# Optimization experiments

Measured on AMD Instinct MI355X. Metric: run time of the kernel, lower is better.

Reference implementation:

```python
import jax, jax.numpy as jnp
import numpy as np

LN_EPS = 1e-5

def _layer_norm(x, gamma, beta):
    mu = jnp.mean(x, axis=-1, keepdims=True)
    var = jnp.mean(jnp.square(x - mu), axis=-1, keepdims=True)
    return (x - mu) * jax.lax.rsqrt(var + LN_EPS) * gamma + beta

def setup_inputs() -> dict:
    key = jax.random.key(0)
    ks = jax.random.split(key, 10)
    B, S, D_IN = 8, 2048, 1024
    H1, H2, C = 2048, 1024, 64
    s1 = 1.0 / np.sqrt(D_IN)
    s2 = 1.0 / np.sqrt(H1)
    s3 = 1.0 / np.sqrt(H2)
    return {
        "embeddings": jax.random.normal(ks[0], (B, S, D_IN), jnp.float32),
        "prior_evidence": jax.random.normal(ks[1], (B, C), jnp.float32),
        "W1": jax.random.uniform(ks[2], (D_IN, H1), jnp.float32, -s1, s1),
        "b1": jnp.zeros((H1,), jnp.float32),
        "g1": jnp.ones((H1,), jnp.float32),
        "beta1": jnp.zeros((H1,), jnp.float32),
        "W2": jax.random.uniform(ks[3], (H1, H2), jnp.float32, -s2, s2),
        "b2": jnp.zeros((H2,), jnp.float32),
        "g2": jnp.ones((H2,), jnp.float32),
        "beta2": jnp.zeros((H2,), jnp.float32),
        "Wh": jax.random.uniform(ks[4], (H2, C), jnp.float32, -s3, s3),
        "bh": jnp.zeros((C,), jnp.float32),
        "and_gate": jnp.ones((C,), jnp.float32),
        "or_gate": jnp.ones((C,), jnp.float32),
    }

def reference(embeddings, prior_evidence, W1, b1, g1, beta1, W2, b2, g2, beta2, Wh, bh, and_gate, or_gate):
    # feature extractor: Linear -> ReLU -> Dropout(eval: identity) -> LayerNorm, x2
    h = _layer_norm(jax.nn.relu(embeddings @ W1 + b1), g1, beta1)
    features = _layer_norm(jax.nn.relu(h @ W2 + b2), g2, beta2)  # [B,S,H2]
    d = features.shape[-1]
    scores = jnp.einsum('bsd,btd->bst', features, features) / jnp.sqrt(jnp.float32(d))
    attention_weights = jax.nn.softmax(scores, axis=-1)          # [B,S,S]
    attended = jnp.einsum('bst,btd->bsd', attention_weights, features)
    logits = attended @ Wh + bh                                   # [B,S,C]
    sig_l = jax.nn.sigmoid(logits)
    sig_p = jax.nn.sigmoid(prior_evidence)[:, None, :]            # [B,1,C] broadcasts
    and_ev = jnp.minimum(sig_l, sig_p) * and_gate
    or_ev = jnp.maximum(sig_l, sig_p) * or_gate
    logits = jnp.log((and_ev + or_ev) / 2 + 1e-10)
    return (logits, attention_weights)
```

## Files before the change

### kernel.cpp

```cpp
#include <hip/hip_runtime.h>

typedef unsigned short u16;
typedef __bf16 bf16x8 __attribute__((ext_vector_type(8)));
typedef float f32x4 __attribute__((ext_vector_type(4)));

__device__ __forceinline__ u16 f2bf(float f) {
    unsigned u = __float_as_uint(f);
    u = (u + 0x7FFFu + ((u >> 16) & 1u)) >> 16;
    return (u16)u;
}
__device__ __forceinline__ float bf2f(u16 h) {
    return __uint_as_float(((unsigned)h) << 16);
}

__device__ __forceinline__ void gld16(const u16* g, u16* l) {
    __builtin_amdgcn_global_load_lds((const __attribute__((address_space(1))) void*)g,
                                     (__attribute__((address_space(3))) void*)l, 16, 0, 0);
}

__device__ __forceinline__ int swz(int row, int col) {
    return ((row >> 4) * 2 + (col >> 5)) * 512 + (row & 15) * 32 +
           ((col & 31) ^ ((row & 8) ? 16 : 0));
}

__global__ __launch_bounds__(256) void cvt_kernel(const float* __restrict__ in,
                                                  u16* __restrict__ out, long n) {
    long i = ((long)blockIdx.x * blockDim.x + threadIdx.x) * 4;
    if (i + 3 < n) {
        float4 v = *(const float4*)&in[i];
        __align__(8) u16 r[4] = {f2bf(v.x), f2bf(v.y), f2bf(v.z), f2bf(v.w)};
        *(int2*)&out[i] = *(const int2*)r;
    }
}

template <int INF32>
__global__ __launch_bounds__(256) void transpose_to_bf16(const void* __restrict__ in,
                                                         u16* __restrict__ out, int R, int C,
                                                         long inB, long outB) {
    __shared__ float tile[32][33];
    const long zi = (long)blockIdx.z * inB;
    const long zo = (long)blockIdx.z * outB;
    const int c0 = blockIdx.x * 32, r0 = blockIdx.y * 32;
    const int tx = threadIdx.x & 31;
    const int ty = threadIdx.x >> 5;
#pragma unroll
    for (int i = 0; i < 32; i += 8) {
        long idx = zi + (long)(r0 + ty + i) * C + c0 + tx;
        float v = INF32 ? ((const float*)in)[idx] : bf2f(((const u16*)in)[idx]);
        tile[ty + i][tx] = v;
    }
    __syncthreads();
#pragma unroll
    for (int i = 0; i < 32; i += 8) {
        out[zo + (long)(c0 + ty + i) * R + r0 + tx] = f2bf(tile[tx][ty + i]);
    }
}

template <int OUTBF>
__global__ __launch_bounds__(512, 2) void gemm_nt(const u16* __restrict__ A,
                                                  const u16* __restrict__ Bm,
                                                  void* __restrict__ Cout, int M, int N, int K,
                                                  long sA, long sB, long sC,
                                                  const float* __restrict__ bias, int relu,
                                                  float scale, int symm) {
    int bx, by, zz;
    if (symm) {
        const int q = gridDim.x >> 3;
        const int orig = blockIdx.x;
        const int wgid = (orig & 7) * q + (orig >> 3);
        const int NB = N >> 8;
        const int nTri = (NB * (NB + 1)) >> 1;
        zz = wgid / nTri;
        int t = wgid - zz * nTri;
        by = 0;
        int rem = NB;
        while (t >= rem) {
            t -= rem;
            --rem;
            ++by;
        }
        bx = by + t;
    } else {
        const int nx = gridDim.x;
        const int nwg = nx * gridDim.y;
        const int orig = blockIdx.y * nx + blockIdx.x;
        const int q = nwg >> 3, r = nwg & 7, xcd = orig & 7, o8 = orig >> 3;
        const int wgid = (xcd < r ? xcd * (q + 1) : r * (q + 1) + (xcd - r) * q) + o8;
        bx = wgid % nx;
        by = wgid / nx;
        zz = blockIdx.z;
    }

    __shared__ __align__(16) u16 As[2][256 * 64];
    __shared__ __align__(16) u16 Bs[2][256 * 64];
    const int tid = threadIdx.x;
    const int lane = tid & 63;
    const int wid = tid >> 6;
    const int wr = wid >> 2;
    const int wc = wid & 3;
    const int l15 = lane & 15, lg = lane >> 4;
    const long zA = (long)zz * sA;
    const long zB = (long)zz * sB;
    const long zC = (long)zz * sC;
    const int m0 = by * 256, n0 = bx * 256;
    const u16* Ab = A + zA + (long)m0 * K;
    const u16* Bb = Bm + zB + (long)n0 * K;
    const int nt = K >> 6;

    f32x4 acc[8][4] = {};

    auto stage = [&](int t, int b) {
#pragma unroll
        for (int i = 0; i < 4; ++i) {
            const int c = i * 512 + tid;
            const int s = c >> 6, r = (c >> 2) & 15;
            const int row = (s >> 1) * 16 + r;
            const int col = (s & 1) * 32 + (((c & 3) * 8) ^ ((r & 8) ? 16 : 0));
            gld16(Ab + (long)row * K + t * 64 + col, &As[b][c * 8]);
        }
#pragma unroll
        for (int i = 0; i < 4; ++i) {
            const int c = i * 512 + tid;
            const int s = c >> 6, r = (c >> 2) & 15;
            const int row = (s >> 1) * 16 + r;
            const int col = (s & 1) * 32 + (((c & 3) * 8) ^ ((r & 8) ? 16 : 0));
            gld16(Bb + (long)row * K + t * 64 + col, &Bs[b][c * 8]);
        }
    };

    stage(0, 0);
    for (int t = 0; t < nt; ++t) {
        const int cur = t & 1;
        if (t + 1 < nt) {
            stage(t + 1, cur ^ 1);
            asm volatile("s_waitcnt vmcnt(8)" ::: "memory");
        } else {
            asm volatile("s_waitcnt vmcnt(0)" ::: "memory");
        }
        __builtin_amdgcn_s_barrier();

        bf16x8 bf[4][2];
#pragma unroll
        for (int n = 0; n < 4; ++n)
#pragma unroll
            for (int kk = 0; kk < 2; ++kk)
                bf[n][kk] = *(const bf16x8*)&Bs[cur][swz(wc * 64 + n * 16 + l15, kk * 32 + lg * 8)];
#pragma unroll
        for (int mg = 0; mg < 4; ++mg) {
            bf16x8 af[2][2];
#pragma unroll
            for (int mi = 0; mi < 2; ++mi)
#pragma unroll
                for (int kk = 0; kk < 2; ++kk)
                    af[mi][kk] = *(const bf16x8*)&As[cur][swz(
                        wr * 128 + mg * 32 + mi * 16 + l15, kk * 32 + lg * 8)];
            __builtin_amdgcn_s_setprio(1);
#pragma unroll
            for (int mi = 0; mi < 2; ++mi)
#pragma unroll
                for (int n = 0; n < 4; ++n)
#pragma unroll
                    for (int kk = 0; kk < 2; ++kk)
                        acc[mg * 2 + mi][n] = __builtin_amdgcn_mfma_f32_16x16x32_bf16(
                            af[mi][kk], bf[n][kk], acc[mg * 2 + mi][n], 0, 0, 0);
            __builtin_amdgcn_s_setprio(0);
            __builtin_amdgcn_s_barrier();
        }
    }

#pragma unroll
    for (int n = 0; n < 4; ++n) {
        const int col = n0 + wc * 64 + n * 16 + l15;
        const float bv = bias ? bias[col] : 0.0f;
#pragma unroll
        for (int m = 0; m < 8; ++m) {
            const int rowb = m0 + wr * 128 + m * 16 + lg * 4;
            float v[4];
#pragma unroll
            for (int r = 0; r < 4; ++r) {
                float f = acc[m][n][r] * scale + bv;
                if (relu) f = fmaxf(f, 0.0f);
                v[r] = f;
                if (OUTBF)
                    ((u16*)Cout)[zC + (long)(rowb + r) * N + col] = f2bf(f);
                else
                    ((float*)Cout)[zC + (long)(rowb + r) * N + col] = f;
            }
            if (!OUTBF && symm && bx > by) {
                *(float4*)&((float*)Cout)[zC + (long)col * N + rowb] =
                    make_float4(v[0], v[1], v[2], v[3]);
            }
        }
    }
}

template <int CH>
__global__ __launch_bounds__(256) void ln_wave(u16* __restrict__ x, const float* __restrict__ g,
                                               const float* __restrict__ be) {
    const int lane = threadIdx.x & 63;
    const int wid = threadIdx.x >> 6;
    const long row = (long)blockIdx.x * 4 + wid;
    u16* p = x + row * (CH * 512);
    __align__(16) u16 raw[CH][8];
    float s = 0.f, ss = 0.f;
#pragma unroll
    for (int c = 0; c < CH; ++c) {
        *(int4*)raw[c] = *(const int4*)&p[(c * 64 + lane) * 8];
#pragma unroll
        for (int j = 0; j < 8; ++j) {
            float f = bf2f(raw[c][j]);
            s += f;
            ss += f * f;
        }
    }
#pragma unroll
    for (int o = 1; o < 64; o <<= 1) {
        s += __shfl_xor(s, o);
        ss += __shfl_xor(ss, o);
    }
    const float inv = 1.0f / (float)(CH * 512);
    const float mu = s * inv;
    const float var = ss * inv - mu * mu;
    const float rs = rsqrtf(var + 1e-5f);
#pragma unroll
    for (int c = 0; c < CH; ++c) {
        const int base = (c * 64 + lane) * 8;
        float4 g0 = *(const float4*)&g[base];
        float4 g1 = *(const float4*)&g[base + 4];
        float4 b0 = *(const float4*)&be[base];
        float4 b1 = *(const float4*)&be[base + 4];
        float gv[8] = {g0.x, g0.y, g0.z, g0.w, g1.x, g1.y, g1.z, g1.w};
        float bv[8] = {b0.x, b0.y, b0.z, b0.w, b1.x, b1.y, b1.z, b1.w};
#pragma unroll
        for (int j = 0; j < 8; ++j)
            raw[c][j] = f2bf((bf2f(raw[c][j]) - mu) * rs * gv[j] + bv[j]);
        *(int4*)&p[base] = *(const int4*)raw[c];
    }
}

__global__ __launch_bounds__(256) void softmax_wave(float* __restrict__ a,
                                                    u16* __restrict__ ab) {
    const int lane = threadIdx.x & 63;
    const int wid = threadIdx.x >> 6;
    const long row = (long)blockIdx.x * 4 + wid;
    float* p = a + row * 2048;
    float v[4][8];
    float mx = -3.4e38f;
#pragma unroll
    for (int c = 0; c < 4; ++c) {
        const int base = (c * 64 + lane) * 8;
        *(float4*)&v[c][0] = *(const float4*)&p[base];
        *(float4*)&v[c][4] = *(const float4*)&p[base + 4];
#pragma unroll
        for (int j = 0; j < 8; ++j) mx = fmaxf(mx, v[c][j]);
    }
#pragma unroll
    for (int o = 1; o < 64; o <<= 1) mx = fmaxf(mx, __shfl_xor(mx, o));
    float s = 0.f;
#pragma unroll
    for (int c = 0; c < 4; ++c)
#pragma unroll
        for (int j = 0; j < 8; ++j) {
            v[c][j] = expf(v[c][j] - mx);
            s += v[c][j];
        }
#pragma unroll
    for (int o = 1; o < 64; o <<= 1) s += __shfl_xor(s, o);
    const float inv = 1.0f / s;
#pragma unroll
    for (int c = 0; c < 4; ++c) {
        const int base = (c * 64 + lane) * 8;
        __align__(16) u16 rb[8];
#pragma unroll
        for (int j = 0; j < 8; ++j) {
            v[c][j] *= inv;
            rb[j] = f2bf(v[c][j]);
        }
        *(float4*)&p[base] = *(const float4*)&v[c][0];
        *(float4*)&p[base + 4] = *(const float4*)&v[c][4];
        *(int4*)&ab[row * 2048 + base] = *(const int4*)rb;
    }
}

__global__ __launch_bounds__(256) void head_kernel(const u16* __restrict__ A,
                                                   const u16* __restrict__ WhT,
                                                   const float* __restrict__ bh,
                                                   const float* __restrict__ prior,
                                                   const float* __restrict__ ag,
                                                   const float* __restrict__ og,
                                                   float* __restrict__ out) {
    __shared__ __align__(16) u16 As2[128 * 64];
    __shared__ __align__(16) u16 Bs2[64 * 64];
    const int tid = threadIdx.x;
    const int lane = tid & 63;
    const int wid = tid >> 6;
    const int l15 = lane & 15, lg = lane >> 4;
    const int m0 = blockIdx.x * 128;
    const int srow = tid >> 3, scol = (tid & 7) * 8;
    const u16* pa = A + (long)(m0 + srow) * 1024 + scol;
    const u16* pb = WhT + (long)srow * 1024 + scol;

    f32x4 acc[2][4] = {};
    for (int k0 = 0; k0 < 1024; k0 += 64) {
#pragma unroll
        for (int i = 0; i < 4; ++i) gld16(pa + (long)i * 32 * 1024 + k0, &As2[i * 2048 + tid * 8]);
#pragma unroll
        for (int i = 0; i < 2; ++i) gld16(pb + (long)i * 32 * 1024 + k0, &Bs2[i * 2048 + tid * 8]);
        __syncthreads();
#pragma unroll
        for (int kk = 0; kk < 2; ++kk) {
            bf16x8 af[2], bfr[4];
#pragma unroll
            for (int m = 0; m < 2; ++m)
                af[m] = *(const bf16x8*)&As2[(wid * 32 + m * 16 + l15) * 64 + kk * 32 + lg * 8];
#pragma unroll
            for (int n = 0; n < 4; ++n)
                bfr[n] = *(const bf16x8*)&Bs2[(n * 16 + l15) * 64 + kk * 32 + lg * 8];
#pragma unroll
            for (int m = 0; m < 2; ++m)
#pragma unroll
                for (int n = 0; n < 4; ++n)
                    acc[m][n] =
                        __builtin_amdgcn_mfma_f32_16x16x32_bf16(af[m], bfr[n], acc[m][n], 0, 0, 0);
        }
        __syncthreads();
    }

#pragma unroll
    for (int n = 0; n < 4; ++n) {
        const int col = n * 16 + l15;
        const float bhv = bh[col];
        const float agv = ag[col];
        const float ogv = og[col];
#pragma unroll
        for (int m = 0; m < 2; ++m) {
#pragma unroll
            for (int r = 0; r < 4; ++r) {
                const int row = m0 + wid * 32 + m * 16 + lg * 4 + r;
                const float logit = acc[m][n][r] + bhv;
                const int b = row >> 11;
                const float sp = 1.f / (1.f + expf(-prior[b * 64 + col]));
                const float sl = 1.f / (1.f + expf(-logit));
                const float av = fminf(sl, sp) * agv;
                const float ov = fmaxf(sl, sp) * ogv;
                out[(long)row * 64 + col] = logf((av + ov) * 0.5f + 1e-10f);
            }
        }
    }
}

extern "C" void kernel_launch(void* const* d_in, const int* in_sizes, int n_in, void* d_out,
                              int out_size, void* d_ws, size_t ws_size, hipStream_t stream) {
    const float* emb = (const float*)d_in[0];
    const float* prior = (const float*)d_in[1];
    const float* W1 = (const float*)d_in[2];
    const float* b1 = (const float*)d_in[3];
    const float* g1 = (const float*)d_in[4];
    const float* be1 = (const float*)d_in[5];
    const float* W2 = (const float*)d_in[6];
    const float* b2 = (const float*)d_in[7];
    const float* g2 = (const float*)d_in[8];
    const float* be2 = (const float*)d_in[9];
    const float* Wh = (const float*)d_in[10];
    const float* bh = (const float*)d_in[11];
    const float* ag = (const float*)d_in[12];
    const float* og = (const float*)d_in[13];

    const int Bn = 8, S = 2048, DIN = 1024, H1 = 2048, H2 = 1024, Cc = 64;
    const int M = Bn * S;

    char* ws = (char*)d_ws;
    size_t off = 0;
    auto alloc = [&](size_t b) {
        size_t o = off;
        off += (b + 255) & ~(size_t)255;
        return o;
    };
    char* R0 = ws + alloc((size_t)M * H1 * 2);
    char* R1 = ws + alloc((size_t)M * DIN * 2);
    char* R2 = ws + alloc((size_t)M * H2 * 2);
    u16* W1t = (u16*)(ws + alloc((size_t)H1 * DIN * 2));
    u16* W2t = (u16*)(ws + alloc((size_t)H2 * H1 * 2));
    u16* WhT = (u16*)(ws + alloc((size_t)Cc * H2 * 2));

    u16* h = (u16*)R0;
    u16* attnb = (u16*)R0;
    u16* embb = (u16*)R1;
    u16* featT = (u16*)R1;
    u16* feat = (u16*)R2;
    u16* attd = (u16*)R2;

    float* out_logits = (float*)d_out;
    float* out_attn = out_logits + (size_t)M * Cc;

    cvt_kernel<<<(int)(((long)M * DIN) / 1024), 256, 0, stream>>>(emb, embb, (long)M * DIN);
    transpose_to_bf16<1><<<dim3(H1 / 32, DIN / 32, 1), 256, 0, stream>>>(W1, W1t, DIN, H1, 0, 0);
    transpose_to_bf16<1><<<dim3(H2 / 32, H1 / 32, 1), 256, 0, stream>>>(W2, W2t, H1, H2, 0, 0);
    transpose_to_bf16<1><<<dim3(Cc / 32, H2 / 32, 1), 256, 0, stream>>>(Wh, WhT, H2, Cc, 0, 0);
    gemm_nt<1><<<dim3(H1 / 256, M / 256, 1), 512, 0, stream>>>(embb, W1t, h, M, H1, DIN, 0, 0, 0,
                                                               b1, 1, 1.0f, 0);
    ln_wave<4><<<M / 4, 256, 0, stream>>>(h, g1, be1);
    gemm_nt<1><<<dim3(H2 / 256, M / 256, 1), 512, 0, stream>>>(h, W2t, feat, M, H2, H1, 0, 0, 0,
                                                               b2, 1, 1.0f, 0);
    ln_wave<2><<<M / 4, 256, 0, stream>>>(feat, g2, be2);
    transpose_to_bf16<0><<<dim3(H2 / 32, S / 32, Bn), 256, 0, stream>>>(
        feat, featT, S, H2, (long)S * H2, (long)H2 * S);
    {
        const int NB = S / 256;
        const int nTri = NB * (NB + 1) / 2;
        gemm_nt<0><<<dim3(nTri * Bn, 1, 1), 512, 0, stream>>>(
            feat, feat, out_attn, S, S, H2, (long)S * H2, (long)S * H2, (long)S * S, nullptr, 0,
            0.03125f, 1);
    }
    softmax_wave<<<M / 4, 256, 0, stream>>>(out_attn, attnb);
    gemm_nt<1><<<dim3(H2 / 256, S / 256, Bn), 512, 0, stream>>>(attnb, featT, attd, S, H2, S,
                                                                (long)S * S, (long)H2 * S,
                                                                (long)S * H2, nullptr, 0, 1.0f,
                                                                0);
    head_kernel<<<M / 128, 256, 0, stream>>>(attd, WhT, bh, prior, ag, og, out_logits);
}
```

Before: 513.4 us.

## Interleave global-to-LDS staging with MFMA groups and double-buffer A fragments

Restructures the GEMM main loop so the next tile's global-to-LDS loads are issued in chunks between MFMA groups, instead of all at once before the compute. A fragments for the next m-group are prefetched from LDS while the current group's MFMAs run. The per-mgroup barriers are removed and two barriers per k-tile are kept around the buffer swap. This aims to hide load latency and LDS read latency behind matrix math, at the cost of more registers and a tighter vmcnt accounting that must stay correct.

```diff
diff --git a/kernel.cpp b/kernel.cpp
--- a/kernel.cpp
+++ b/kernel.cpp
@@ -109,63 +109,70 @@
 
     f32x4 acc[8][4] = {};
 
-    auto stage = [&](int t, int b) {
-#pragma unroll
-        for (int i = 0; i < 4; ++i) {
-            const int c = i * 512 + tid;
-            const int s = c >> 6, r = (c >> 2) & 15;
-            const int row = (s >> 1) * 16 + r;
-            const int col = (s & 1) * 32 + (((c & 3) * 8) ^ ((r & 8) ? 16 : 0));
-            gld16(Ab + (long)row * K + t * 64 + col, &As[b][c * 8]);
-        }
-#pragma unroll
-        for (int i = 0; i < 4; ++i) {
-            const int c = i * 512 + tid;
-            const int s = c >> 6, r = (c >> 2) & 15;
-            const int row = (s >> 1) * 16 + r;
-            const int col = (s & 1) * 32 + (((c & 3) * 8) ^ ((r & 8) ? 16 : 0));
-            gld16(Bb + (long)row * K + t * 64 + col, &Bs[b][c * 8]);
-        }
+    auto stage_chunk = [&](int t, int b, int j) {
+        const int c = j * 512 + tid;
+        const int s = c >> 6, r = (c >> 2) & 15;
+        const int row = (s >> 1) * 16 + r;
+        const int col = (s & 1) * 32 + (((c & 3) * 8) ^ ((r & 8) ? 16 : 0));
+        gld16(Ab + (long)row * K + t * 64 + col, &As[b][c * 8]);
+        gld16(Bb + (long)row * K + t * 64 + col, &Bs[b][c * 8]);
     };
 
-    stage(0, 0);
+#pragma unroll
+    for (int j = 0; j < 4; ++j) stage_chunk(0, 0, j);
+    if (nt > 1) {
+        stage_chunk(1, 1, 0);
+        asm volatile("s_waitcnt vmcnt(2)" ::: "memory");
+    } else {
+        asm volatile("s_waitcnt vmcnt(0)" ::: "memory");
+    }
+    __builtin_amdgcn_s_barrier();
+
     for (int t = 0; t < nt; ++t) {
         const int cur = t & 1;
-        if (t + 1 < nt) {
-            stage(t + 1, cur ^ 1);
-            asm volatile("s_waitcnt vmcnt(8)" ::: "memory");
+        bf16x8 bf[4][2];
+#pragma unroll
+        for (int n = 0; n < 4; ++n)
+#pragma unroll
+            for (int kk = 0; kk < 2; ++kk)
+                bf[n][kk] = *(const bf16x8*)&Bs[cur][swz(wc * 64 + n * 16 + l15, kk * 32 + lg * 8)];
+        bf16x8 af[2][2][2];
+#pragma unroll
+        for (int mi = 0; mi < 2; ++mi)
+#pragma unroll
+            for (int kk = 0; kk < 2; ++kk)
+                af[0][mi][kk] =
+                    *(const bf16x8*)&As[cur][swz(wr * 128 + mi * 16 + l15, kk * 32 + lg * 8)];
+#pragma unroll
+        for (int mg = 0; mg < 4; ++mg) {
+            if (mg < 3) {
+#pragma unroll
+                for (int mi = 0; mi < 2; ++mi)
+#pragma unroll
+                    for (int kk = 0; kk < 2; ++kk)
+                        af[(mg + 1) & 1][mi][kk] = *(const bf16x8*)&As[cur][swz(
+                            wr * 128 + (mg + 1) * 32 + mi * 16 + l15, kk * 32 + lg * 8)];
+                if (t + 1 < nt) stage_chunk(t + 1, cur ^ 1, mg + 1);
+            }
+            __builtin_amdgcn_s_setprio(1);
+#pragma unroll
+            for (int mi = 0; mi < 2; ++mi)
+#pragma unroll
+                for (int n = 0; n < 4; ++n)
+#pragma unroll
+                    for (int kk = 0; kk < 2; ++kk)
+                        acc[mg * 2 + mi][n] = __builtin_amdgcn_mfma_f32_16x16x32_bf16(
+                            af[mg & 1][mi][kk], bf[n][kk], acc[mg * 2 + mi][n], 0, 0, 0);
+            __builtin_amdgcn_s_setprio(0);
+        }
+        __builtin_amdgcn_s_barrier();
+        if (t + 2 < nt) {
+            stage_chunk(t + 2, cur, 0);
+            asm volatile("s_waitcnt vmcnt(2)" ::: "memory");
         } else {
             asm volatile("s_waitcnt vmcnt(0)" ::: "memory");
         }
         __builtin_amdgcn_s_barrier();
-
-        bf16x8 bf[4][2];
-#pragma unroll
-        for (int n = 0; n < 4; ++n)
-#pragma unroll
-            for (int kk = 0; kk < 2; ++kk)
-                bf[n][kk] = *(const bf16x8*)&Bs[cur][swz(wc * 64 + n * 16 + l15, kk * 32 + lg * 8)];
-#pragma unroll
-        for (int mg = 0; mg < 4; ++mg) {
-            bf16x8 af[2][2];
-#pragma unroll
-            for (int mi = 0; mi < 2; ++mi)
-#pragma unroll
-                for (int kk = 0; kk < 2; ++kk)
-                    af[mi][kk] = *(const bf16x8*)&As[cur][swz(
-                        wr * 128 + mg * 32 + mi * 16 + l15, kk * 32 + lg * 8)];
-            __builtin_amdgcn_s_setprio(1);
-#pragma unroll
-            for (int mi = 0; mi < 2; ++mi)
-#pragma unroll
-                for (int n = 0; n < 4; ++n)
-#pragma unroll
-                    for (int kk = 0; kk < 2; ++kk)
-                        acc[mg * 2 + mi][n] = __builtin_amdgcn_mfma_f32_16x16x32_bf16(
-                            af[mi][kk], bf[n][kk], acc[mg * 2 + mi][n], 0, 0, 0);
-            __builtin_amdgcn_s_setprio(0);
-            __builtin_amdgcn_s_barrier();
-        }
     }
 
 #pragma unroll
```

After: 488.6 us. 4.8% less time.

## Restructure GEMM mainloop into 4-stage K=32 pipeline with split staging

Applied to the files above, without the earlier changes.

The GEMM's double-buffered K=64 mainloop becomes a 4-buffer ring of K=32 slices, prefetched three iterations ahead. Global-to-LDS loads for each future slice are split into two halves interleaved between the two MFMA phases. The XOR swizzle is dropped in favour of a plain row-major 32-wide LDS layout. The aim is deeper latency hiding and finer interleaving of loads with MFMA work, at the cost of twice as many barriers per unit of K and possible LDS bank conflicts from the unswizzled layout.

```diff
diff --git a/kernel.cpp b/kernel.cpp
--- a/kernel.cpp
+++ b/kernel.cpp
@@ -16,11 +16,6 @@
 __device__ __forceinline__ void gld16(const u16* g, u16* l) {
     __builtin_amdgcn_global_load_lds((const __attribute__((address_space(1))) void*)g,
                                      (__attribute__((address_space(3))) void*)l, 16, 0, 0);
-}
-
-__device__ __forceinline__ int swz(int row, int col) {
-    return ((row >> 4) * 2 + (col >> 5)) * 512 + (row & 15) * 32 +
-           ((col & 31) ^ ((row & 8) ? 16 : 0));
 }
 
 __global__ __launch_bounds__(256) void cvt_kernel(const float* __restrict__ in,
@@ -91,8 +86,8 @@
         zz = blockIdx.z;
     }
 
-    __shared__ __align__(16) u16 As[2][256 * 64];
-    __shared__ __align__(16) u16 Bs[2][256 * 64];
+    __shared__ __align__(16) u16 As[4][256 * 32];
+    __shared__ __align__(16) u16 Bs[4][256 * 32];
     const int tid = threadIdx.x;
     const int lane = tid & 63;
     const int wid = tid >> 6;
@@ -105,67 +100,77 @@
     const int m0 = by * 256, n0 = bx * 256;
     const u16* Ab = A + zA + (long)m0 * K;
     const u16* Bb = Bm + zB + (long)n0 * K;
-    const int nt = K >> 6;
+    const int nt = K >> 5;
 
     f32x4 acc[8][4] = {};
 
-    auto stage = [&](int t, int b) {
-#pragma unroll
-        for (int i = 0; i < 4; ++i) {
-            const int c = i * 512 + tid;
-            const int s = c >> 6, r = (c >> 2) & 15;
-            const int row = (s >> 1) * 16 + r;
-            const int col = (s & 1) * 32 + (((c & 3) * 8) ^ ((r & 8) ? 16 : 0));
-            gld16(Ab + (long)row * K + t * 64 + col, &As[b][c * 8]);
-        }
-#pragma unroll
-        for (int i = 0; i < 4; ++i) {
-            const int c = i * 512 + tid;
-            const int s = c >> 6, r = (c >> 2) & 15;
-            const int row = (s >> 1) * 16 + r;
-            const int col = (s & 1) * 32 + (((c & 3) * 8) ^ ((r & 8) ? 16 : 0));
-            gld16(Bb + (long)row * K + t * 64 + col, &Bs[b][c * 8]);
-        }
+    auto stage_chunk = [&](int x, int j) {
+        const int b = x & 3;
+        const int c = j * 512 + tid;
+        const int r = c >> 2, g = c & 3;
+        const long co = (long)x * 32 + g * 8;
+        gld16(Ab + (long)r * K + co, &As[b][c * 8]);
+        gld16(Bb + (long)r * K + co, &Bs[b][c * 8]);
     };
 
-    stage(0, 0);
+#pragma unroll
+    for (int x = 0; x < 3; ++x) {
+        stage_chunk(x, 0);
+        stage_chunk(x, 1);
+    }
+    asm volatile("s_waitcnt vmcnt(8)" ::: "memory");
+    __builtin_amdgcn_s_barrier();
+
     for (int t = 0; t < nt; ++t) {
-        const int cur = t & 1;
-        if (t + 1 < nt) {
-            stage(t + 1, cur ^ 1);
+        const u16* Ac = &As[t & 3][0];
+        const u16* Bc = &Bs[t & 3][0];
+        bf16x8 bf[4], af[4];
+#pragma unroll
+        for (int n = 0; n < 4; ++n)
+            bf[n] = *(const bf16x8*)&Bc[(wc * 64 + n * 16 + l15) * 32 + lg * 8];
+#pragma unroll
+        for (int m = 0; m < 4; ++m)
+            af[m] = *(const bf16x8*)&Ac[(wr * 128 + m * 16 + l15) * 32 + lg * 8];
+        if (t + 3 < nt) stage_chunk(t + 3, 0);
+        __builtin_amdgcn_sched_barrier(0);
+        __builtin_amdgcn_s_barrier();
+        asm volatile("s_waitcnt lgkmcnt(0)" ::: "memory");
+        __builtin_amdgcn_sched_barrier(0);
+        __builtin_amdgcn_s_setprio(1);
+#pragma unroll
+        for (int m = 0; m < 4; ++m)
+#pragma unroll
+            for (int n = 0; n < 4; ++n)
+                acc[m][n] =
+                    __builtin_amdgcn_mfma_f32_16x16x32_bf16(af[m], bf[n], acc[m][n], 0, 0, 0);
+        __builtin_amdgcn_s_setprio(0);
+        __builtin_amdgcn_sched_barrier(0);
+        __builtin_amdgcn_s_barrier();
+#pragma unroll
+        for (int m = 0; m < 4; ++m)
+            af[m] = *(const bf16x8*)&Ac[(wr * 128 + 64 + m * 16 + l15) * 32 + lg * 8];
+        if (t + 3 < nt) stage_chunk(t + 3, 1);
+        __builtin_amdgcn_sched_barrier(0);
+        __builtin_amdgcn_s_barrier();
+        asm volatile("s_waitcnt lgkmcnt(0)" ::: "memory");
+        __builtin_amdgcn_sched_barrier(0);
+        __builtin_amdgcn_s_setprio(1);
+#pragma unroll
+        for (int m = 0; m < 4; ++m)
+#pragma unroll
+            for (int n = 0; n < 4; ++n)
+                acc[4 + m][n] = __builtin_amdgcn_mfma_f32_16x16x32_bf16(af[m], bf[n],
+                                                                        acc[4 + m][n], 0, 0, 0);
+        __builtin_amdgcn_s_setprio(0);
+        if (t + 3 < nt) {
             asm volatile("s_waitcnt vmcnt(8)" ::: "memory");
-        } else {
+        } else if (t + 2 < nt) {
+            asm volatile("s_waitcnt vmcnt(4)" ::: "memory");
+        } else if (t + 1 < nt) {
             asm volatile("s_waitcnt vmcnt(0)" ::: "memory");
         }
+        __builtin_amdgcn_sched_barrier(0);
         __builtin_amdgcn_s_barrier();
-
-        bf16x8 bf[4][2];
-#pragma unroll
-        for (int n = 0; n < 4; ++n)
-#pragma unroll
-            for (int kk = 0; kk < 2; ++kk)
-                bf[n][kk] = *(const bf16x8*)&Bs[cur][swz(wc * 64 + n * 16 + l15, kk * 32 + lg * 8)];
-#pragma unroll
-        for (int mg = 0; mg < 4; ++mg) {
-            bf16x8 af[2][2];
-#pragma unroll
-            for (int mi = 0; mi < 2; ++mi)
-#pragma unroll
-                for (int kk = 0; kk < 2; ++kk)
-                    af[mi][kk] = *(const bf16x8*)&As[cur][swz(
-                        wr * 128 + mg * 32 + mi * 16 + l15, kk * 32 + lg * 8)];
-            __builtin_amdgcn_s_setprio(1);
-#pragma unroll
-            for (int mi = 0; mi < 2; ++mi)
-#pragma unroll
-                for (int n = 0; n < 4; ++n)
-#pragma unroll
-                    for (int kk = 0; kk < 2; ++kk)
-                        acc[mg * 2 + mi][n] = __builtin_amdgcn_mfma_f32_16x16x32_bf16(
-                            af[mi][kk], bf[n][kk], acc[mg * 2 + mi][n], 0, 0, 0);
-            __builtin_amdgcn_s_setprio(0);
-            __builtin_amdgcn_s_barrier();
-        }
     }
 
 #pragma unroll
```

After: 502.7 us. 2.1% less time.
